# Performance work log

Hardware: AMD Instinct MI355X
Metric: run time of the kernel (lower is better)

## Reference

```python
import jax, jax.numpy as jnp
import numpy as np

N_COG = 72  # 360 / delta_cog
N_RB = 72   # 360 / delta_rb
B, N, H = 64, 512, 128


def setup_inputs() -> dict:
    key = jax.random.key(0)
    k1, k2, k3, k4, k5, k6 = jax.random.split(key, 6)
    h_t = jax.random.normal(k1, (N, B, H), dtype=jnp.float32)
    r_mat = jax.random.randint(k2, (B, N, N), 0, N_RB, dtype=jnp.int32)
    d_mat = jax.random.uniform(k3, (B, N, N), dtype=jnp.float32)
    mask = jax.random.randint(k4, (B, N), 0, 2).astype(jnp.float32)
    cog_mat = jax.random.randint(k5, (B, N, N), 0, N_COG, dtype=jnp.int32)
    domain = jax.random.normal(k6, (N_COG, N_RB), dtype=jnp.float32)
    return {"h_t": h_t, "r_mat": r_mat, "d_mat": d_mat, "mask": mask,
            "cog_mat": cog_mat, "domain": domain}


def reference(h_t, r_mat, d_mat, mask, cog_mat, domain):
    # gather from learnable domain table, subtract distance, relu
    w = jax.nn.relu(domain[cog_mat, r_mat] - d_mat)          # [B, N, N]
    # pairwise mask (applied twice in the original, around normalization)
    m = mask[:, :, None] * mask[:, None, :]                   # [B, N, N]
    w = m * w
    # global-max normalize; torch uses .data.max() (no grad through max)
    w = w / jax.lax.stop_gradient(jnp.max(w))
    w = m * w
    # out[b,i,h] = sum_j w[b,i,j] * h_t[j,b,h]
    return jnp.einsum('bij,jbh->bih', w, h_t)                 # [B, N, H]
```

## Files before the change

kernel.cpp:

```cpp
#include <hip/hip_runtime.h>


#define B_   64
#define N_   512
#define H_   128
#define NCOG 72
#define NRB  72

typedef __bf16 bf16x8 __attribute__((ext_vector_type(8)));
typedef float  f32x4  __attribute__((ext_vector_type(4)));

__device__ __forceinline__ void async_copy16_nt(const void* g, void* l) {
    __builtin_amdgcn_global_load_lds(
        (const __attribute__((address_space(1))) void*)g,
        (__attribute__((address_space(3))) void*)l, 16, 0, 2);
}

__global__ __launch_bounds__(256) void k_transpose(const float* __restrict__ ht,
                                                   __bf16* __restrict__ T) {
    __shared__ __bf16 tile[32][136];
    const int jt = blockIdx.x * 32;
    const int b  = blockIdx.y;
    const int t  = threadIdx.x;
    {
        const int jj = t >> 3;
        const int h0 = (t & 7) << 4;
        const float* src = ht + ((size_t)(jt + jj) * B_ + b) * H_ + h0;
        float4 v0 = *(const float4*)(src + 0);
        float4 v1 = *(const float4*)(src + 4);
        float4 v2 = *(const float4*)(src + 8);
        float4 v3 = *(const float4*)(src + 12);
        __bf16* dst = &tile[jj][h0];
        dst[0]=(__bf16)v0.x; dst[1]=(__bf16)v0.y; dst[2]=(__bf16)v0.z; dst[3]=(__bf16)v0.w;
        dst[4]=(__bf16)v1.x; dst[5]=(__bf16)v1.y; dst[6]=(__bf16)v1.z; dst[7]=(__bf16)v1.w;
        dst[8]=(__bf16)v2.x; dst[9]=(__bf16)v2.y; dst[10]=(__bf16)v2.z; dst[11]=(__bf16)v2.w;
        dst[12]=(__bf16)v3.x; dst[13]=(__bf16)v3.y; dst[14]=(__bf16)v3.z; dst[15]=(__bf16)v3.w;
    }
    __syncthreads();
    {
        const int h  = t >> 1;
        const int j0 = (t & 1) << 4;
        union { bf16x8 v[2]; __bf16 e[16]; } ob;
        #pragma unroll
        for (int q = 0; q < 16; ++q) ob.e[q] = tile[j0 + q][h];
        __bf16* dst = T + ((size_t)b * H_ + h) * N_ + jt + j0;
        *(bf16x8*)(dst + 0) = ob.v[0];
        *(bf16x8*)(dst + 8) = ob.v[1];
    }
}

__global__ __launch_bounds__(512, 1) void k_main(const int* __restrict__ cog,
                                                 const int* __restrict__ rmat,
                                                 const float* __restrict__ dmat,
                                                 const float* __restrict__ mask,
                                                 const float* __restrict__ domain,
                                                 const __bf16* __restrict__ T,
                                                 float* __restrict__ out,
                                                 unsigned int* __restrict__ gmax) {
    __shared__ int   tiles[4 * 3 * 2048];
    __shared__ float sdom[NCOG * NRB];
    __shared__ float smask[N_];
    __shared__ float swmax[8];

    const int id    = blockIdx.x;
    const int xcd   = id & 7;
    const int i0idx = (id >> 3) & 7;
    const int bhi   = id >> 6;
    const int b     = xcd + 8 * bhi;
    const int i0    = i0idx * 64;
    const int kstart = (id & 15) * 32;

    const int t    = threadIdx.x;
    const int wave = t >> 6;
    const int lane = t & 63;

    for (int k = t; k < NCOG * NRB; k += 512) sdom[k] = domain[k];
    for (int k = t; k < N_; k += 512) smask[k] = mask[b * N_ + k];

    const size_t robase = ((size_t)b * N_ + i0) * N_;

    float wmax = 0.0f;

    if (wave >= 4) {
        const int pw   = wave - 4;
        const int csw4 = ((lane & 7) ^ (lane >> 3)) * 4;
        const size_t poff = (size_t)(lane >> 3) * N_ + csw4;

        #define ISSUE_BATCH(n)                                                      \
            do {                                                                    \
                const int kk_ = (kstart + (n) * 32) & (N_ - 1);                     \
                const int buf_ = (n) & 3;                                           \
                _Pragma("unroll")                                                   \
                for (int q6 = 0; q6 < 6; ++q6) {                                    \
                    const int q = pw * 6 + q6, a = q >> 3, c8 = q & 7;              \
                    const size_t goff = robase + (size_t)(c8 * 8) * N_ + kk_ + poff;\
                    const void* g = (a == 0) ? (const void*)(cog + goff)            \
                                  : (a == 1) ? (const void*)(rmat + goff)           \
                                             : (const void*)(dmat + goff);         \
                    async_copy16_nt(g, &tiles[buf_ * 6144 + a * 2048 + c8 * 256]);  \
                }                                                                   \
            } while (0)

        ISSUE_BATCH(0);
        ISSUE_BATCH(1);
        ISSUE_BATCH(2);
        asm volatile("s_waitcnt vmcnt(12) lgkmcnt(0)\n\ts_barrier" ::: "memory");

        for (int s = 0; s < 16; ++s) {
            if (s < 13) {
                ISSUE_BATCH(s + 3);
                asm volatile("s_waitcnt vmcnt(12)\n\ts_barrier" ::: "memory");
            } else if (s == 13) {
                asm volatile("s_waitcnt vmcnt(6)\n\ts_barrier" ::: "memory");
            } else if (s == 14) {
                asm volatile("s_waitcnt vmcnt(0)\n\ts_barrier" ::: "memory");
            } else {
                asm volatile("s_barrier" ::: "memory");
            }
        }
        #undef ISSUE_BATCH
    } else {
        const int quad = lane >> 4;
        const int lrow = lane & 15;
        const int row  = wave * 16 + lrow;
        const int g0   = (row * 8 + ((quad * 2)     ^ (row & 7))) * 4;
        const int g1   = (row * 8 + ((quad * 2 + 1) ^ (row & 7))) * 4;
        const __bf16* Tcol = T + (size_t)b * H_ * N_ + (size_t)lrow * N_ + quad * 8;

        f32x4 acc[8];
        #pragma unroll
        for (int i = 0; i < 8; ++i) acc[i] = (f32x4)0.0f;

        bf16x8 bfbuf[2][8];
        #pragma unroll
        for (int nt = 0; nt < 8; ++nt)
            bfbuf[0][nt] = *(const bf16x8*)(Tcol + (size_t)nt * 16 * N_ + kstart);

        __syncthreads();
        #pragma unroll 4
        for (int s = 0; s < 16; ++s) {
            const int kk  = (kstart + s * 32) & (N_ - 1);
            const int cb  = s & 1;
            if (s + 1 < 16) {
                const int kk2 = (kstart + s * 32 + 32) & (N_ - 1);
                #pragma unroll
                for (int nt = 0; nt < 8; ++nt)
                    bfbuf[cb ^ 1][nt] = *(const bf16x8*)(Tcol + (size_t)nt * 16 * N_ + kk2);
            }
            const int jb = kk + quad * 8;
            const int* tb = tiles + (s & 3) * 6144;
            union { int4 v[2]; int   e[8]; } ci, ri;
            union { int4 v[2]; float e[8]; } di;
            ci.v[0] = *(const int4*)(tb + g0);        ci.v[1] = *(const int4*)(tb + g1);
            ri.v[0] = *(const int4*)(tb + 2048 + g0); ri.v[1] = *(const int4*)(tb + 2048 + g1);
            di.v[0] = *(const int4*)(tb + 4096 + g0); di.v[1] = *(const int4*)(tb + 4096 + g1);

            union { bf16x8 v8; __bf16 e[8]; } af;
            #pragma unroll
            for (int q = 0; q < 8; ++q) {
                float val = sdom[ci.e[q] * NRB + ri.e[q]] - di.e[q];
                val = fmaxf(val, 0.0f) * smask[jb + q];
                wmax = fmaxf(wmax, val);
                af.e[q] = (__bf16)val;
            }
            #pragma unroll
            for (int nt = 0; nt < 8; ++nt)
                acc[nt] = __builtin_amdgcn_mfma_f32_16x16x32_bf16(af.v8, bfbuf[cb][nt], acc[nt], 0, 0, 0);
            __syncthreads();
        }

        wmax *= smask[i0 + row];

        const int orow0 = i0 + wave * 16 + quad * 4;
        #pragma unroll
        for (int nt = 0; nt < 8; ++nt) {
            #pragma unroll
            for (int r = 0; r < 4; ++r)
                out[((size_t)b * N_ + orow0 + r) * H_ + nt * 16 + lrow] = acc[nt][r];
        }
    }

    #pragma unroll
    for (int off = 32; off > 0; off >>= 1)
        wmax = fmaxf(wmax, __shfl_down(wmax, off));
    if (lane == 0) swmax[wave] = wmax;
    __syncthreads();
    if (t == 0) {
        float m = swmax[0];
        #pragma unroll
        for (int w = 1; w < 8; ++w) m = fmaxf(m, swmax[w]);
        atomicMax(gmax, __float_as_uint(m));
    }
}

__global__ __launch_bounds__(256) void k_scale(float* __restrict__ out,
                                               const float* __restrict__ mask,
                                               const unsigned int* __restrict__ gmax) {
    const float inv = 1.0f / __uint_as_float(*gmax);
    const int idx = blockIdx.x * 256 + threadIdx.x;
    const float m = mask[idx >> 5] * inv;
    float4* p = (float4*)out;
    float4 v = p[idx];
    v.x *= m; v.y *= m; v.z *= m; v.w *= m;
    p[idx] = v;
}

extern "C" void kernel_launch(void* const* d_in, const int* in_sizes, int n_in,
                              void* d_out, int out_size, void* d_ws, size_t ws_size,
                              hipStream_t stream) {
    const float* ht     = (const float*)d_in[0];
    const int*   rmat   = (const int*)  d_in[1];
    const float* dmat   = (const float*)d_in[2];
    const float* mask   = (const float*)d_in[3];
    const int*   cog    = (const int*)  d_in[4];
    const float* domain = (const float*)d_in[5];
    float* out = (float*)d_out;

    unsigned int* gmax = (unsigned int*)d_ws;
    __bf16* T = (__bf16*)((char*)d_ws + 256);

    hipMemsetAsync(d_ws, 0, 256, stream);
    k_transpose<<<dim3(16, 64), 256, 0, stream>>>(ht, T);
    k_main<<<dim3(512), 512, 0, stream>>>(cog, rmat, dmat, mask, domain, T, out, gmax);
    k_scale<<<4096, 256, 0, stream>>>(out, mask, gmax);
}
```

Baseline: 230.3 us.

## Replace async global-to-LDS copies with register-staged loads and double-buffered LDS

The producer waves now load the cog, r and d tiles into registers with nontemporal global loads and then write them to LDS, where before they copied directly from global memory into LDS. LDS is cut from four stages to two, and the launch bounds now allow several blocks per CU. The goal is to raise occupancy and give the compiler control over the loads. The cost is a shallower prefetch pipeline, an extra register-to-LDS store step, and more register pressure in the producer waves.

```diff
diff --git a/kernel.cpp b/kernel.cpp
--- a/kernel.cpp
+++ b/kernel.cpp
@@ -9,12 +9,7 @@
 
 typedef __bf16 bf16x8 __attribute__((ext_vector_type(8)));
 typedef float  f32x4  __attribute__((ext_vector_type(4)));
-
-__device__ __forceinline__ void async_copy16_nt(const void* g, void* l) {
-    __builtin_amdgcn_global_load_lds(
-        (const __attribute__((address_space(1))) void*)g,
-        (__attribute__((address_space(3))) void*)l, 16, 0, 2);
-}
+typedef unsigned int u32x4 __attribute__((ext_vector_type(4)));
 
 __global__ __launch_bounds__(256) void k_transpose(const float* __restrict__ ht,
                                                    __bf16* __restrict__ T) {
@@ -49,7 +44,7 @@
     }
 }
 
-__global__ __launch_bounds__(512, 1) void k_main(const int* __restrict__ cog,
+__global__ __launch_bounds__(512, 4) void k_main(const int* __restrict__ cog,
                                                  const int* __restrict__ rmat,
                                                  const float* __restrict__ dmat,
                                                  const float* __restrict__ mask,
@@ -57,7 +52,7 @@
                                                  const __bf16* __restrict__ T,
                                                  float* __restrict__ out,
                                                  unsigned int* __restrict__ gmax) {
-    __shared__ int   tiles[4 * 3 * 2048];
+    __shared__ int   tiles[2 * 3 * 2048];
     __shared__ float sdom[NCOG * NRB];
     __shared__ float smask[N_];
     __shared__ float swmax[8];
@@ -82,43 +77,52 @@
     float wmax = 0.0f;
 
     if (wave >= 4) {
-        const int pw   = wave - 4;
-        const int csw4 = ((lane & 7) ^ (lane >> 3)) * 4;
-        const size_t poff = (size_t)(lane >> 3) * N_ + csw4;
-
-        #define ISSUE_BATCH(n)                                                      \
-            do {                                                                    \
-                const int kk_ = (kstart + (n) * 32) & (N_ - 1);                     \
-                const int buf_ = (n) & 3;                                           \
-                _Pragma("unroll")                                                   \
-                for (int q6 = 0; q6 < 6; ++q6) {                                    \
-                    const int q = pw * 6 + q6, a = q >> 3, c8 = q & 7;              \
-                    const size_t goff = robase + (size_t)(c8 * 8) * N_ + kk_ + poff;\
-                    const void* g = (a == 0) ? (const void*)(cog + goff)            \
-                                  : (a == 1) ? (const void*)(rmat + goff)           \
-                                             : (const void*)(dmat + goff);         \
-                    async_copy16_nt(g, &tiles[buf_ * 6144 + a * 2048 + c8 * 256]);  \
-                }                                                                   \
+        const int pw = wave - 4;
+        const int r  = lane >> 3;
+        const int c  = lane & 7;
+        const size_t gl_off = (size_t)r * N_ + c * 4;
+        const int    ds_off = r * 32 + ((c ^ r) << 2);
+
+        u32x4 regs[2][6];
+
+        #define LOAD_BATCH(n, set)                                                   \
+            do {                                                                     \
+                const int kk_ = (kstart + (n) * 32) & (N_ - 1);                      \
+                _Pragma("unroll")                                                    \
+                for (int q6 = 0; q6 < 6; ++q6) {                                     \
+                    const int q = pw * 6 + q6, a = q >> 3, c8 = q & 7;               \
+                    const size_t goff = robase + (size_t)(c8 * 8) * N_ + kk_ + gl_off;\
+                    const unsigned int* g = (a == 0) ? (const unsigned int*)cog      \
+                                           : (a == 1) ? (const unsigned int*)rmat    \
+                                                      : (const unsigned int*)dmat;   \
+                    regs[set][q6] = __builtin_nontemporal_load((const u32x4*)(g + goff)); \
+                }                                                                    \
             } while (0)
 
-        ISSUE_BATCH(0);
-        ISSUE_BATCH(1);
-        ISSUE_BATCH(2);
-        asm volatile("s_waitcnt vmcnt(12) lgkmcnt(0)\n\ts_barrier" ::: "memory");
-
+        #define STORE_BATCH(n, set)                                                  \
+            do {                                                                     \
+                const int buf_ = (n) & 1;                                            \
+                _Pragma("unroll")                                                    \
+                for (int q6 = 0; q6 < 6; ++q6) {                                     \
+                    const int q = pw * 6 + q6, a = q >> 3, c8 = q & 7;               \
+                    *(u32x4*)&tiles[buf_ * 6144 + a * 2048 + c8 * 256 + ds_off] = regs[set][q6]; \
+                }                                                                    \
+            } while (0)
+
+        LOAD_BATCH(0, 0);
+        LOAD_BATCH(1, 1);
+        STORE_BATCH(0, 0);
+        asm volatile("s_waitcnt lgkmcnt(0)\n\ts_barrier" ::: "memory");
+
+        #pragma unroll
         for (int s = 0; s < 16; ++s) {
-            if (s < 13) {
-                ISSUE_BATCH(s + 3);
-                asm volatile("s_waitcnt vmcnt(12)\n\ts_barrier" ::: "memory");
-            } else if (s == 13) {
-                asm volatile("s_waitcnt vmcnt(6)\n\ts_barrier" ::: "memory");
-            } else if (s == 14) {
-                asm volatile("s_waitcnt vmcnt(0)\n\ts_barrier" ::: "memory");
-            } else {
-                asm volatile("s_barrier" ::: "memory");
-            }
+            if (s < 14) LOAD_BATCH(s + 2, s & 1);
+            __builtin_amdgcn_sched_barrier(0);
+            if (s < 15) STORE_BATCH(s + 1, (s + 1) & 1);
+            asm volatile("s_waitcnt lgkmcnt(0)\n\ts_barrier" ::: "memory");
         }
-        #undef ISSUE_BATCH
+        #undef LOAD_BATCH
+        #undef STORE_BATCH
     } else {
         const int quad = lane >> 4;
         const int lrow = lane & 15;
@@ -148,7 +152,7 @@
                     bfbuf[cb ^ 1][nt] = *(const bf16x8*)(Tcol + (size_t)nt * 16 * N_ + kk2);
             }
             const int jb = kk + quad * 8;
-            const int* tb = tiles + (s & 3) * 6144;
+            const int* tb = tiles + (s & 1) * 6144;
             union { int4 v[2]; int   e[8]; } ci, ri;
             union { int4 v[2]; float e[8]; } di;
             ci.v[0] = *(const int4*)(tb + g0);        ci.v[1] = *(const int4*)(tb + g1);
```

After: 244.1 us. +6.0%, slower.
